# Kernel optimization log

Measured on AMD Instinct MI355X. Metric: run time of the kernel, lower is better.

## Reference

```python
import jax, jax.numpy as jnp
import numpy as np

DIM = 96
NHEAD = 8
HEAD_DIM = DIM // NHEAD  # 12
N, L, S = 1, 262144, 262144  # 64^3 flattened 3D volume tokens
EPS_LA = 1e-6
EPS_LN = 1e-5


def layer_norm(x, w, b):
    mu = jnp.mean(x, axis=-1, keepdims=True)
    var = jnp.mean((x - mu) ** 2, axis=-1, keepdims=True)
    return (x - mu) * jax.lax.rsqrt(var + EPS_LN) * w + b


def setup_inputs() -> dict:
    key = jax.random.key(0)
    ks = jax.random.split(key, 24)
    std = 0.02
    def w(k, shape):
        return jax.random.normal(k, shape, dtype=jnp.float32) * std
    inp = {
        "mr_seg_feat_flatten": jax.random.normal(ks[0], (N, L, DIM), dtype=jnp.float32),
        "ct2mr_attention_flatten": jax.random.normal(ks[1], (N, L, DIM), dtype=jnp.float32),
        "warp_ctfeat": jax.random.normal(ks[2], (N, S, DIM), dtype=jnp.float32),
        # CrossmodalSemanticsCalibration params (torch Linear weights: [out, in])
        "w_qkv": w(ks[3], (DIM, DIM)),
        "w_qkv2": w(ks[4], (DIM, DIM)),
        "ln1_w": jnp.ones((DIM,), jnp.float32),
        "ln1_b": jnp.zeros((DIM,), jnp.float32),
        "ln2_w": jnp.ones((2 * DIM,), jnp.float32),
        "ln2_b": jnp.zeros((2 * DIM,), jnp.float32),
        "mlp_fc1_w": w(ks[5], (2 * DIM, 2 * DIM)),
        "mlp_fc1_b": jnp.zeros((2 * DIM,), jnp.float32),
        "mlp_fc2_w": w(ks[6], (DIM, 2 * DIM)),
        "mlp_fc2_b": jnp.zeros((DIM,), jnp.float32),
        # StructureAttention(96, 8) params
        "sa_wq": w(ks[7], (DIM, DIM)),
        "sa_wk": w(ks[8], (DIM, DIM)),
        "sa_wv": w(ks[9], (DIM, DIM)),
        "sa_merge": w(ks[10], (DIM, DIM)),
        "sa_mlp_w1": w(ks[11], (2 * DIM, 2 * DIM)),
        "sa_mlp_w2": w(ks[12], (DIM, 2 * DIM)),
        "sa_ln1_w": jnp.ones((DIM,), jnp.float32),
        "sa_ln1_b": jnp.zeros((DIM,), jnp.float32),
        "sa_ln2_w": jnp.ones((DIM,), jnp.float32),
        "sa_ln2_b": jnp.zeros((DIM,), jnp.float32),
    }
    return inp


def _forward(mr_seg_feat_flatten, ct2mr_attention_flatten, warp_ctfeat,
             w_qkv, w_qkv2, ln1_w, ln1_b, ln2_w, ln2_b,
             mlp_fc1_w, mlp_fc1_b, mlp_fc2_w, mlp_fc2_b,
             sa_wq, sa_wk, sa_wv, sa_merge, sa_mlp_w1, sa_mlp_w2,
             sa_ln1_w, sa_ln1_b, sa_ln2_w, sa_ln2_b):
    # CrossmodalSemanticsCalibration.forward (ct2mr_attention_flatten is unused, as in torch)
    x0 = layer_norm(mr_seg_feat_flatten, ln1_w, ln1_b)
    shortcut = x0 @ w_qkv.T                        # [N, L, C]
    y = shortcut @ w_qkv2.T                        # [N, L, C]

    # StructureAttention(y, warp_ctfeat) with kernelized LinearAttention
    n, l, c = y.shape
    s = warp_ctfeat.shape[1]
    q = (y @ sa_wq.T).reshape(n, l, NHEAD, HEAD_DIM)
    k = (warp_ctfeat @ sa_wk.T).reshape(n, s, NHEAD, HEAD_DIM)
    v = (warp_ctfeat @ sa_wv.T).reshape(n, s, NHEAD, HEAD_DIM)
    Q = jax.nn.elu(q) + 1.0
    K = jax.nn.elu(k) + 1.0
    KV = jnp.einsum('nshd,nshv->nhdv', K, v / s)   # [N, H, d, d]
    Z = 1.0 / (jnp.einsum('nlhd,nhd->nlh', Q, K.sum(axis=1)) + EPS_LA)
    msg = jnp.einsum('nlhd,nhdv,nlh->nlhv', Q, KV, Z) * s
    msg = msg.reshape(n, l, c) @ sa_merge.T
    msg = layer_norm(msg, sa_ln1_w, sa_ln1_b)
    h = jnp.concatenate([y, msg], axis=-1) @ sa_mlp_w1.T
    h = jax.nn.relu(h) @ sa_mlp_w2.T
    h = layer_norm(h, sa_ln2_w, sa_ln2_b)
    x = y + h                                      # StructureAttention output

    # fuse with shortcut, final Mlp (GELU, exact erf as torch default)
    x = jnp.concatenate([x, shortcut], axis=-1)    # [N, L, 2C]
    x = layer_norm(x, ln2_w, ln2_b)
    x = jax.nn.gelu(x @ mlp_fc1_w.T + mlp_fc1_b, approximate=False)
    x = x @ mlp_fc2_w.T + mlp_fc2_b
    return x                                       # [N, L, C]


def reference(mr_seg_feat_flatten, ct2mr_attention_flatten, warp_ctfeat,
              w_qkv, w_qkv2, ln1_w, ln1_b, ln2_w, ln2_b,
              mlp_fc1_w, mlp_fc1_b, mlp_fc2_w, mlp_fc2_b,
              sa_wq, sa_wk, sa_wv, sa_merge, sa_mlp_w1, sa_mlp_w2,
              sa_ln1_w, sa_ln1_b, sa_ln2_w, sa_ln2_b):
    return _forward(mr_seg_feat_flatten, ct2mr_attention_flatten, warp_ctfeat,
                    w_qkv, w_qkv2, ln1_w, ln1_b, ln2_w, ln2_b,
                    mlp_fc1_w, mlp_fc1_b, mlp_fc2_w, mlp_fc2_b,
                    sa_wq, sa_wk, sa_wv, sa_merge, sa_mlp_w1, sa_mlp_w2,
                    sa_ln1_w, sa_ln1_b, sa_ln2_w, sa_ln2_b)
```

## Files before the change

### kernel.cpp

```cpp
#include <hip/hip_runtime.h>
#include <hip/hip_bf16.h>


typedef __attribute__((ext_vector_type(8))) short short8;
typedef __attribute__((ext_vector_type(4))) float f32x4;
typedef __attribute__((ext_vector_type(4))) unsigned int uint4v;

#define WS_FLAG 0
#define WS_PKV  512
#define WS_PSV  (WS_PKV + 16*9216*4)
#define WS_PSE  (WS_PSV + 16*96*4)
#define WS_KSUM (WS_PSE + 16*96*4)
#define WS_KSTOT (WS_KSUM + 96*4)
#define WS_CM   (WS_KSTOT + 64)
#define WS_BDT  (WS_CM + 768*4)
#define WS_WB   (WS_BDT + 9216*2)
#define WS_VEC  (WS_WB + 165888*2)

#define OQKV   0
#define OQKV2  9216
#define OWQ    18432
#define OWK    27648
#define OWV    36864
#define OMERGE 46080
#define OW1    55296
#define OW2    92160
#define OFC1   110592
#define OFC2   147456
#define VLN1W 0
#define VLN1B 96
#define VLN2W 192
#define VLN2B 384
#define VFC1B 576
#define VFC2B 768
#define VSA1W 864
#define VSA1B 960
#define VSA2W 1056
#define VSA2B 1152

struct InPtrs { const void* p[23]; };

__device__ inline float b2f(unsigned short x) {
  union { unsigned u; float f; } c; c.u = ((unsigned)x) << 16; return c.f;
}
__device__ inline unsigned short f2b(float f) {
  __hip_bfloat16 h = __float2bfloat16(f);
  return *(unsigned short*)&h;
}
__device__ inline uint2 pack4bf(float v0, float v1, float v2, float v3) {
  uint2 r;
  r.x = (unsigned)f2b(v0) | ((unsigned)f2b(v1) << 16);
  r.y = (unsigned)f2b(v2) | ((unsigned)f2b(v3) << 16);
  return r;
}

__global__ void probe_k(const void* in0, unsigned* flag) {
  int tid = threadIdx.x;
  const unsigned short* u = (const unsigned short*)in0;
  int cnt = 0;
  for (int j = 0; j < 8; ++j) {
    unsigned short v = u[(tid * 8 + j) * 2];
    unsigned e = (v >> 7) & 0xFF;
    if ((e >= 110 && e <= 141) || ((v & 0x7FFF) == 0)) cnt++;
  }
  for (int o = 32; o; o >>= 1) cnt += __shfl_down(cnt, o);
  if (tid == 0) *flag = (cnt > 256) ? 1u : 0u;
}

template<int ISBF>
__launch_bounds__(256)
__global__ void prep_k(InPtrs ip, char* ws) {
  if (((const unsigned*)ws)[0] != (unsigned)ISBF) return;
  const int wsrc[10] = {3,4,13,14,15,16,17,18,9,11};
  const int wdst[11] = {0,9216,18432,27648,36864,46080,55296,92160,110592,147456,165888};
  const int vsrc[10] = {5,6,7,8,10,12,19,20,21,22};
  const int vdst[11] = {0,96,192,384,576,768,864,960,1056,1152,1248};
  unsigned short* wb = (unsigned short*)(ws + WS_WB);
  float* vec = (float*)(ws + WS_VEC);
  float* zr = (float*)(ws + WS_PKV);
  const int TOT = 165888 + 1248 + 150528;
  for (int e = blockIdx.x * 256 + threadIdx.x; e < TOT; e += gridDim.x * 256) {
    if (e < 165888) {
      int w = 0;
      while (w < 9 && e >= wdst[w + 1]) ++w;
      int loc = e - wdst[w];
      if (ISBF) wb[e] = ((const unsigned short*)ip.p[wsrc[w]])[loc];
      else      wb[e] = f2b(((const float*)ip.p[wsrc[w]])[loc]);
    } else if (e < 165888 + 1248) {
      int e2 = e - 165888;
      int w = 0;
      while (w < 9 && e2 >= vdst[w + 1]) ++w;
      int loc = e2 - vdst[w];
      vec[e2] = ISBF ? b2f(((const unsigned short*)ip.p[vsrc[w]])[loc])
                     : ((const float*)ip.p[vsrc[w]])[loc];
    } else {
      zr[e - 165888 - 1248] = 0.0f;
    }
  }
}

template<int NB, int NCF, int KSTEPS>
__device__ inline void domm(const unsigned short* A, int apitch,
                            const unsigned short* B, int bpitch, int cf0,
                            int lane, f32x4 (&acc)[NB][NCF]) {
  int lr = lane & 15, lg = lane >> 4;
#pragma unroll
  for (int ks = 0; ks < KSTEPS; ++ks) {
    int k0 = ks * 32 + lg * 8;
    short8 bf[NCF];
#pragma unroll
    for (int cf = 0; cf < NCF; ++cf)
      bf[cf] = *(const short8*)(B + ((cf0 + cf) * 16 + lr) * bpitch + k0);
    short8 af[NB];
#pragma unroll
    for (int b = 0; b < NB; ++b)
      af[b] = *(const short8*)(A + (b * 16 + lr) * apitch + k0);
#pragma unroll
    for (int cf = 0; cf < NCF; ++cf)
#pragma unroll
      for (int b = 0; b < NB; ++b)
        acc[b][cf] = __builtin_amdgcn_mfma_f32_16x16x32_bf16(af[b], bf[cf], acc[b][cf], 0, 0, 0);
  }
}

template<int NB, int NCF>
__device__ inline void writeFrags(unsigned short* dst, int pitch, int cf0,
                                  int lane, f32x4 (&acc)[NB][NCF]) {
  int lr = lane & 15, lg = lane >> 4;
#pragma unroll
  for (int b = 0; b < NB; ++b)
#pragma unroll
    for (int cf = 0; cf < NCF; ++cf)
#pragma unroll
      for (int r = 0; r < 4; ++r) {
        float v = acc[b][cf][r];
        float v1 = __shfl_xor(v, 1);
        float v2 = __shfl_xor(v, 2);
        float v3 = __shfl_xor(v, 3);
        if ((lane & 3) == 0) {
          int row = b * 16 + lg * 4 + r;
          int col = (cf0 + cf) * 16 + lr;
          *(uint2*)(dst + row * pitch + col) = pack4bf(v, v1, v2, v3);
        }
      }
}

template<int NB, int NCF>
__device__ inline void zacc(f32x4 (&acc)[NB][NCF]) {
#pragma unroll
  for (int b = 0; b < NB; ++b)
#pragma unroll
    for (int cf = 0; cf < NCF; ++cf)
      acc[b][cf] = (f32x4){0.f, 0.f, 0.f, 0.f};
}

template<int ISBF>
__launch_bounds__(256)
__global__ void kA(const void* ct_, char* ws) {
  if (((const unsigned*)ws)[0] != (unsigned)ISBF) return;
  __shared__ unsigned short sCT[64][104];
  __shared__ unsigned short sEK[96][72];
  __shared__ unsigned short sVT[96][72];
  const unsigned short* Wb = (const unsigned short*)(ws + WS_WB);
  float* pKV = (float*)(ws + WS_PKV);
  int tid = threadIdx.x, lane = tid & 63, wid = tid >> 6;
  int lr = lane & 15, lg = lane >> 4;

  f32x4 kvacc[2][6];
  zacc<2, 6>(kvacc);
  float accEk = 0.f, accV = 0.f;

  for (int t = blockIdx.x; t < 4096; t += gridDim.x) {
    if (ISBF) {
      const uint4v* src = (const uint4v*)((const unsigned short*)ct_ + (size_t)t * 6144);
#pragma unroll
      for (int i = 0; i < 3; ++i) {
        int ch = tid * 3 + i;
        int r = ch / 12, c = (ch % 12) * 8;
        *(uint4v*)&sCT[r][c] = src[ch];
      }
    } else {
      const float4* src = (const float4*)((const float*)ct_ + (size_t)t * 6144);
#pragma unroll
      for (int i = 0; i < 6; ++i) {
        int ch = tid * 6 + i;
        int r = ch / 24, c = (ch % 24) * 4;
        float4 v = src[ch];
        *(uint2*)&sCT[r][c] = pack4bf(v.x, v.y, v.z, v.w);
      }
    }
    __syncthreads();

    const unsigned short* Wp = Wb + ((wid < 2) ? OWK : OWV);
    int cf0 = (wid & 1) * 3;
    f32x4 pacc[4][3];
    zacc<4, 3>(pacc);
    domm<4, 3, 3>(&sCT[0][0], 104, Wp, 96, cf0, lane, pacc);
    if (wid < 2) {
#pragma unroll
      for (int b = 0; b < 4; ++b)
#pragma unroll
        for (int cf = 0; cf < 3; ++cf)
#pragma unroll
          for (int r = 0; r < 4; ++r) {
            float v = pacc[b][cf][r];
            pacc[b][cf][r] = v > 0.f ? v : expm1f(v);
          }
    }
    {
      unsigned short* dstT = (wid < 2) ? &sEK[0][0] : &sVT[0][0];
#pragma unroll
      for (int b = 0; b < 4; ++b)
#pragma unroll
        for (int cf = 0; cf < 3; ++cf) {
          int col = (cf0 + cf) * 16 + lr;
          int t0 = b * 16 + lg * 4;
          *(uint2*)(dstT + col * 72 + t0) =
              pack4bf(pacc[b][cf][0], pacc[b][cf][1], pacc[b][cf][2], pacc[b][cf][3]);
        }
    }
    __syncthreads();

    if (wid < 3) {
#pragma unroll
      for (int ks = 0; ks < 2; ++ks) {
        int k0 = ks * 32 + lg * 8;
        short8 a[2];
#pragma unroll
        for (int bb = 0; bb < 2; ++bb)
          a[bb] = *(const short8*)&sEK[(wid * 2 + bb) * 16 + lr][k0];
#pragma unroll
        for (int cf = 0; cf < 6; ++cf) {
          short8 vb = *(const short8*)&sVT[cf * 16 + lr][k0];
#pragma unroll
          for (int bb = 0; bb < 2; ++bb)
            kvacc[bb][cf] = __builtin_amdgcn_mfma_f32_16x16x32_bf16(a[bb], vb, kvacc[bb][cf], 0, 0, 0);
        }
      }
    }
    if (tid < 96) {
#pragma unroll
      for (int j = 0; j < 8; ++j) {
        short8 e = *(const short8*)&sEK[tid][j * 8];
        short8 v = *(const short8*)&sVT[tid][j * 8];
#pragma unroll
        for (int q = 0; q < 8; ++q) {
          accEk += b2f((unsigned short)e[q]);
          accV  += b2f((unsigned short)v[q]);
        }
      }
    }
    __syncthreads();
  }

  int slice = blockIdx.x & 15;
  if (tid < 96) {
    atomicAdd((float*)(ws + WS_PSE) + slice * 96 + tid, accEk);
    atomicAdd((float*)(ws + WS_PSV) + slice * 96 + tid, accV);
  }
  if (wid < 3) {
#pragma unroll
    for (int bb = 0; bb < 2; ++bb)
#pragma unroll
      for (int cf = 0; cf < 6; ++cf)
#pragma unroll
        for (int r = 0; r < 4; ++r) {
          int hd = (wid * 2 + bb) * 16 + lg * 4 + r;
          int hv = cf * 16 + lr;
          if (hd / 12 == hv / 12)
            atomicAdd(&pKV[slice * 9216 + hd * 96 + hv], kvacc[bb][cf][r]);
        }
  }
}

template<int ISBF>
__launch_bounds__(256)
__global__ void kFin(const void* merge_, char* ws) {
  if (((const unsigned*)ws)[0] != (unsigned)ISBF) return;
  __shared__ float Ks[96], sV[96], KV[8][12][12], csk[96];
  int tid = threadIdx.x;
  const float* pSE = (const float*)(ws + WS_PSE);
  const float* pSV = (const float*)(ws + WS_PSV);
  const float* pKV = (const float*)(ws + WS_PKV);
  if (tid < 96) {
    float a = 0.f, b = 0.f;
    for (int s = 0; s < 16; ++s) { a += pSE[s * 96 + tid]; b += pSV[s * 96 + tid]; }
    Ks[tid] = 262144.0f + a;
    sV[tid] = b;
    ((float*)(ws + WS_KSUM))[tid] = Ks[tid];
  }
  __syncthreads();
  if (tid < 8) {
    float s = 0.f;
    for (int d = 0; d < 12; ++d) s += Ks[tid * 12 + d];
    ((float*)(ws + WS_KSTOT))[tid] = s;
  }
  for (int e = tid; e < 1152; e += 256) {
    int h = e / 144, r = e % 144, d = r / 12, v = r % 12;
    int hd = h * 12 + d, hv = h * 12 + v;
    float s = sV[hv];
    for (int sl = 0; sl < 16; ++sl) s += pKV[sl * 9216 + hd * 96 + hv];
    KV[h][d][v] = s * (1.0f / 262144.0f);
  }
  unsigned short* bdt = (unsigned short*)(ws + WS_BDT);
  for (int e = tid; e < 9216; e += 256) bdt[e] = 0;
  __syncthreads();
  for (int e = tid; e < 1152; e += 256) {
    int h = e / 144, r = e % 144, d = r / 12, v = r % 12;
    bdt[(h * 12 + v) * 96 + (h * 12 + d)] = f2b(KV[h][d][v]);
  }
  if (tid < 96) {
    int h = tid / 12, v = tid % 12;
    float s = 0.f;
    for (int d = 0; d < 12; ++d) s += KV[h][d][v];
    csk[tid] = s;
  }
  __syncthreads();
  for (int e = tid; e < 768; e += 256) {
    int h = e / 96, c = e % 96;
    float s = 0.f;
    for (int v = 0; v < 12; ++v) {
      float mg = ISBF ? b2f(((const unsigned short*)merge_)[c * 96 + h * 12 + v])
                      : ((const float*)merge_)[c * 96 + h * 12 + v];
      s += csk[h * 12 + v] * mg;
    }
    ((float*)(ws + WS_CM))[e] = s;
  }
}

template<int ISBF>
__launch_bounds__(128)
__global__ void kB(const void* mr_, void* out_, char* ws) {
  if (((const unsigned*)ws)[0] != (unsigned)ISBF) return;
  __shared__ unsigned short sA[64][200];
  __shared__ unsigned short sS[64][104];
  __shared__ unsigned short sY[64][96];
  __shared__ float sZs[64][8];
  const unsigned short* Wb = (const unsigned short*)(ws + WS_WB);
  const float* vec  = (const float*)(ws + WS_VEC);
  const float* Ksum = (const float*)(ws + WS_KSUM);
  const float* KsTot = (const float*)(ws + WS_KSTOT);
  const float* CM = (const float*)(ws + WS_CM);
  const unsigned short* BDT = (const unsigned short*)(ws + WS_BDT);
  int tid = threadIdx.x, lane = tid & 63, wid = tid >> 6;
  int lr = lane & 15, lg = lane >> 4;
  int tok0 = blockIdx.x * 64;

  if (ISBF) {
    const uint4v* src = (const uint4v*)((const unsigned short*)mr_ + (size_t)tok0 * 96);
#pragma unroll
    for (int i = 0; i < 6; ++i) {
      int ch = tid * 6 + i;
      int r = ch / 12, c = (ch % 12) * 8;
      *(uint4v*)&sA[r][c] = src[ch];
    }
  } else {
    const float4* src = (const float4*)((const float*)mr_ + (size_t)tok0 * 96);
#pragma unroll
    for (int i = 0; i < 12; ++i) {
      int ch = tid * 12 + i;
      int r = ch / 24, c = (ch % 24) * 4;
      float4 v = src[ch];
      *(uint2*)&sA[r][c] = pack4bf(v.x, v.y, v.z, v.w);
    }
  }
  __syncthreads();

  int row = tid >> 1, c0 = (tid & 1) * 48;

  {
    float vals[48];
    float s = 0.f, s2 = 0.f;
#pragma unroll
    for (int i = 0; i < 6; ++i) {
      short8 v = *(const short8*)&sA[row][c0 + i * 8];
#pragma unroll
      for (int j = 0; j < 8; ++j) {
        float x = b2f((unsigned short)v[j]);
        vals[i * 8 + j] = x; s += x; s2 += x * x;
      }
    }
    s += __shfl_xor(s, 1); s2 += __shfl_xor(s2, 1);
    float mean = s * (1.f / 96.f);
    float rs = rsqrtf(s2 * (1.f / 96.f) - mean * mean + 1e-5f);
#pragma unroll
    for (int i = 0; i < 6; ++i) {
      short8 o;
#pragma unroll
      for (int j = 0; j < 8; ++j) {
        int c = c0 + i * 8 + j;
        o[j] = (short)f2b((vals[i * 8 + j] - mean) * rs * vec[VLN1W + c] + vec[VLN1B + c]);
      }
      *(short8*)&sA[row][c0 + i * 8] = o;
    }
  }
  __syncthreads();

  f32x4 acc3[4][3];
  f32x4 acc6[4][6];

  zacc<4, 3>(acc3);
  domm<4, 3, 3>(&sA[0][0], 200, Wb + OQKV, 96, wid * 3, lane, acc3);
  writeFrags<4, 3>(&sS[0][0], 104, wid * 3, lane, acc3);
  __syncthreads();

  zacc<4, 3>(acc3);
  domm<4, 3, 3>(&sS[0][0], 104, Wb + OQKV2, 96, wid * 3, lane, acc3);
  writeFrags<4, 3>(&sY[0][0], 96, wid * 3, lane, acc3);
  __syncthreads();

  zacc<4, 3>(acc3);
  domm<4, 3, 3>(&sY[0][0], 96, Wb + OWQ, 96, wid * 3, lane, acc3);
#pragma unroll
  for (int b = 0; b < 4; ++b)
#pragma unroll
    for (int cf = 0; cf < 3; ++cf)
#pragma unroll
      for (int r = 0; r < 4; ++r) {
        float v = acc3[b][cf][r];
        acc3[b][cf][r] = v > 0.f ? v : expm1f(v);
      }
  writeFrags<4, 3>(&sA[0][0], 200, wid * 3, lane, acc3);
  __syncthreads();

#pragma unroll
  for (int i = 0; i < 4; ++i) {
    int task = tid + 128 * i;
    int zr = task >> 3, h = task & 7;
    float den = KsTot[h];
#pragma unroll
    for (int d = 0; d < 12; ++d)
      den += b2f(sA[zr][h * 12 + d]) * Ksum[h * 12 + d];
    sZs[zr][h] = 262144.0f / (den + 1e-6f);
  }
  __syncthreads();

  zacc<4, 3>(acc3);
  domm<4, 3, 3>(&sA[0][0], 200, BDT, 96, wid * 3, lane, acc3);
#pragma unroll
  for (int b = 0; b < 4; ++b)
#pragma unroll
    for (int cf = 0; cf < 3; ++cf) {
      int col = (wid * 3 + cf) * 16 + lr;
      int h = col / 12;
#pragma unroll
      for (int r = 0; r < 4; ++r) {
        int rw = b * 16 + lg * 4 + r;
        acc3[b][cf][r] *= sZs[rw][h];
      }
    }
  writeFrags<4, 3>(&sA[0][96], 200, wid * 3, lane, acc3);
  __syncthreads();

  zacc<4, 3>(acc3);
  domm<4, 3, 3>(&sA[0][96], 200, Wb + OMERGE, 96, wid * 3, lane, acc3);
  writeFrags<4, 3>(&sA[0][0], 200, wid * 3, lane, acc3);
  __syncthreads();

  {
    float vals[48];
#pragma unroll
    for (int j = 0; j < 48; ++j) vals[j] = 0.f;
#pragma unroll
    for (int h = 0; h < 8; ++h) {
      float zh = sZs[row][h];
      const float* cmr = CM + h * 96 + c0;
#pragma unroll
      for (int j = 0; j < 48; j += 4) {
        float4 c4 = *(const float4*)(cmr + j);
        vals[j] += zh * c4.x; vals[j + 1] += zh * c4.y;
        vals[j + 2] += zh * c4.z; vals[j + 3] += zh * c4.w;
      }
    }
    float s = 0.f, s2 = 0.f;
#pragma unroll
    for (int i = 0; i < 6; ++i) {
      short8 v = *(const short8*)&sA[row][c0 + i * 8];
#pragma unroll
      for (int j = 0; j < 8; ++j) {
        float x = vals[i * 8 + j] + b2f((unsigned short)v[j]);
        vals[i * 8 + j] = x; s += x; s2 += x * x;
      }
    }
    s += __shfl_xor(s, 1); s2 += __shfl_xor(s2, 1);
    float mean = s * (1.f / 96.f);
    float rs = rsqrtf(s2 * (1.f / 96.f) - mean * mean + 1e-5f);
#pragma unroll
    for (int i = 0; i < 6; ++i) {
      short8 o;
#pragma unroll
      for (int j = 0; j < 8; ++j) {
        int c = c0 + i * 8 + j;
        o[j] = (short)f2b((vals[i * 8 + j] - mean) * rs * vec[VSA1W + c] + vec[VSA1B + c]);
      }
      *(short8*)&sA[row][96 + c0 + i * 8] = o;
    }
#pragma unroll
    for (int i = 0; i < 6; ++i)
      *(uint4v*)&sA[row][c0 + i * 8] = *(const uint4v*)&sY[row][c0 + i * 8];
  }
  __syncthreads();

  zacc<4, 6>(acc6);
  domm<4, 6, 6>(&sA[0][0], 200, Wb + OW1, 192, wid * 6, lane, acc6);
#pragma unroll
  for (int b = 0; b < 4; ++b)
#pragma unroll
    for (int cf = 0; cf < 6; ++cf)
#pragma unroll
      for (int r = 0; r < 4; ++r)
        acc6[b][cf][r] = fmaxf(acc6[b][cf][r], 0.f);
  __syncthreads();
  writeFrags<4, 6>(&sA[0][0], 200, wid * 6, lane, acc6);
  __syncthreads();

  zacc<4, 3>(acc3);
  domm<4, 3, 6>(&sA[0][0], 200, Wb + OW2, 192, wid * 3, lane, acc3);
  __syncthreads();
  writeFrags<4, 3>(&sA[0][0], 200, wid * 3, lane, acc3);
  __syncthreads();

  {
    float vals[48];
    float s = 0.f, s2 = 0.f;
#pragma unroll
    for (int i = 0; i < 6; ++i) {
      short8 v = *(const short8*)&sA[row][c0 + i * 8];
#pragma unroll
      for (int j = 0; j < 8; ++j) {
        float x = b2f((unsigned short)v[j]);
        vals[i * 8 + j] = x; s += x; s2 += x * x;
      }
    }
    s += __shfl_xor(s, 1); s2 += __shfl_xor(s2, 1);
    float mh = s * (1.f / 96.f);
    float rh = rsqrtf(s2 * (1.f / 96.f) - mh * mh + 1e-5f);
    float sx = 0.f, sx2 = 0.f;
#pragma unroll
    for (int j = 0; j < 48; ++j) {
      int c = c0 + j;
      float x = b2f(sY[row][c]) + (vals[j] - mh) * rh * vec[VSA2W + c] + vec[VSA2B + c];
      vals[j] = x; sx += x; sx2 += x * x;
    }
#pragma unroll
    for (int j = 0; j < 48; ++j) {
      float sv = b2f(sS[row][c0 + j]);
      sx += sv; sx2 += sv * sv;
    }
    sx += __shfl_xor(sx, 1); sx2 += __shfl_xor(sx2, 1);
    float m2 = sx * (1.f / 192.f);
    float r2 = rsqrtf(sx2 * (1.f / 192.f) - m2 * m2 + 1e-5f);
#pragma unroll
    for (int i = 0; i < 6; ++i) {
      short8 o;
#pragma unroll
      for (int j = 0; j < 8; ++j) {
        int c = c0 + i * 8 + j;
        o[j] = (short)f2b((vals[i * 8 + j] - m2) * r2 * vec[VLN2W + c] + vec[VLN2B + c]);
      }
      *(short8*)&sA[row][c0 + i * 8] = o;
    }
#pragma unroll
    for (int i = 0; i < 6; ++i) {
      short8 o;
#pragma unroll
      for (int j = 0; j < 8; ++j) {
        int c = c0 + i * 8 + j;
        float sv = b2f(sS[row][c]);
        o[j] = (short)f2b((sv - m2) * r2 * vec[VLN2W + 96 + c] + vec[VLN2B + 96 + c]);
      }
      *(short8*)&sA[row][96 + c0 + i * 8] = o;
    }
  }
  __syncthreads();

  zacc<4, 6>(acc6);
  domm<4, 6, 6>(&sA[0][0], 200, Wb + OFC1, 192, wid * 6, lane, acc6);
#pragma unroll
  for (int cf = 0; cf < 6; ++cf) {
    float bb = vec[VFC1B + (wid * 6 + cf) * 16 + lr];
#pragma unroll
    for (int b = 0; b < 4; ++b)
#pragma unroll
      for (int r = 0; r < 4; ++r) {
        float x = acc6[b][cf][r] + bb;
        acc6[b][cf][r] = 0.5f * x * (1.0f + erff(x * 0.70710678118f));
      }
  }
  __syncthreads();
  writeFrags<4, 6>(&sA[0][0], 200, wid * 6, lane, acc6);
  __syncthreads();

  zacc<4, 3>(acc3);
  domm<4, 3, 6>(&sA[0][0], 200, Wb + OFC2, 192, wid * 3, lane, acc3);
#pragma unroll
  for (int b = 0; b < 4; ++b)
#pragma unroll
    for (int cf = 0; cf < 3; ++cf)
#pragma unroll
      for (int r = 0; r < 4; ++r) {
        int col = (wid * 3 + cf) * 16 + lr;
        float v = acc3[b][cf][r] + vec[VFC2B + col];
        float v1 = __shfl_xor(v, 1);
        float v2 = __shfl_xor(v, 2);
        float v3 = __shfl_xor(v, 3);
        if ((lane & 3) == 0) {
          size_t token = (size_t)tok0 + b * 16 + lg * 4 + r;
          size_t off = token * 96 + col;
          if (ISBF) {
            *(uint2*)((unsigned short*)out_ + off) = pack4bf(v, v1, v2, v3);
          } else {
            float4 f; f.x = v; f.y = v1; f.z = v2; f.w = v3;
            *(float4*)((float*)out_ + off) = f;
          }
        }
      }
}

extern "C" void kernel_launch(void* const* d_in, const int* in_sizes, int n_in,
                              void* d_out, int out_size, void* d_ws, size_t ws_size,
                              hipStream_t stream) {
  (void)in_sizes; (void)n_in; (void)out_size; (void)ws_size;
  char* ws = (char*)d_ws;
  probe_k<<<1, 64, 0, stream>>>(d_in[0], (unsigned*)ws);
  InPtrs ip;
  for (int i = 0; i < 23; ++i) ip.p[i] = d_in[i];
  prep_k<0><<<512, 256, 0, stream>>>(ip, ws);
  prep_k<1><<<512, 256, 0, stream>>>(ip, ws);
  kA<0><<<1024, 256, 0, stream>>>(d_in[2], ws);
  kA<1><<<1024, 256, 0, stream>>>(d_in[2], ws);
  kFin<0><<<1, 256, 0, stream>>>(d_in[16], ws);
  kFin<1><<<1, 256, 0, stream>>>(d_in[16], ws);
  kB<0><<<4096, 128, 0, stream>>>(d_in[0], d_out, ws);
  kB<1><<<4096, 128, 0, stream>>>(d_in[0], d_out, ws);
}
```

Measured before the change: 765.1 us.

## Split kB token tile across four waves by rows and use 256-thread blocks

Raises kB's block size from 128 to 256 threads, and each wave now owns 16 token rows with all output columns. Before, two waves split the columns over all 64 rows. This should cut per-wave accumulator registers and raise occupancy and latency hiding, at the cost of each wave re-reading the full weight tiles. Layer norms now use a two-pass variance for stability, run on only half the threads, and the final LN output loops are fused.

```diff
diff --git a/kernel.cpp b/kernel.cpp
--- a/kernel.cpp
+++ b/kernel.cpp
@@ -244,9 +244,9 @@
         short8 e = *(const short8*)&sEK[tid][j * 8];
         short8 v = *(const short8*)&sVT[tid][j * 8];
 #pragma unroll
-        for (int q = 0; q < 8; ++q) {
-          accEk += b2f((unsigned short)e[q]);
-          accV  += b2f((unsigned short)v[q]);
+        for (int qq = 0; qq < 8; ++qq) {
+          accEk += b2f((unsigned short)e[qq]);
+          accV  += b2f((unsigned short)v[qq]);
         }
       }
     }
@@ -329,7 +329,7 @@
 }
 
 template<int ISBF>
-__launch_bounds__(128)
+__launch_bounds__(256, 2)
 __global__ void kB(const void* mr_, void* out_, char* ws) {
   if (((const unsigned*)ws)[0] != (unsigned)ISBF) return;
   __shared__ unsigned short sA[64][200];
@@ -344,21 +344,23 @@
   const unsigned short* BDT = (const unsigned short*)(ws + WS_BDT);
   int tid = threadIdx.x, lane = tid & 63, wid = tid >> 6;
   int lr = lane & 15, lg = lane >> 4;
+  int w16 = wid * 16;
+  int row = tid >> 1, c0 = (tid & 1) * 48;
   int tok0 = blockIdx.x * 64;
 
   if (ISBF) {
     const uint4v* src = (const uint4v*)((const unsigned short*)mr_ + (size_t)tok0 * 96);
 #pragma unroll
+    for (int i = 0; i < 3; ++i) {
+      int ch = tid * 3 + i;
+      int r = ch / 12, c = (ch % 12) * 8;
+      *(uint4v*)&sA[r][c] = src[ch];
+    }
+  } else {
+    const float4* src = (const float4*)((const float*)mr_ + (size_t)tok0 * 96);
+#pragma unroll
     for (int i = 0; i < 6; ++i) {
       int ch = tid * 6 + i;
-      int r = ch / 12, c = (ch % 12) * 8;
-      *(uint4v*)&sA[r][c] = src[ch];
-    }
-  } else {
-    const float4* src = (const float4*)((const float*)mr_ + (size_t)tok0 * 96);
-#pragma unroll
-    for (int i = 0; i < 12; ++i) {
-      int ch = tid * 12 + i;
       int r = ch / 24, c = (ch % 24) * 4;
       float4 v = src[ch];
       *(uint2*)&sA[r][c] = pack4bf(v.x, v.y, v.z, v.w);
@@ -366,23 +368,25 @@
   }
   __syncthreads();
 
-  int row = tid >> 1, c0 = (tid & 1) * 48;
-
-  {
+  if (tid < 128) {
     float vals[48];
-    float s = 0.f, s2 = 0.f;
+    float s = 0.f;
 #pragma unroll
     for (int i = 0; i < 6; ++i) {
       short8 v = *(const short8*)&sA[row][c0 + i * 8];
 #pragma unroll
       for (int j = 0; j < 8; ++j) {
         float x = b2f((unsigned short)v[j]);
-        vals[i * 8 + j] = x; s += x; s2 += x * x;
-      }
-    }
-    s += __shfl_xor(s, 1); s2 += __shfl_xor(s2, 1);
+        vals[i * 8 + j] = x; s += x;
+      }
+    }
+    s += __shfl_xor(s, 1);
     float mean = s * (1.f / 96.f);
-    float rs = rsqrtf(s2 * (1.f / 96.f) - mean * mean + 1e-5f);
+    float s2 = 0.f;
+#pragma unroll
+    for (int j = 0; j < 48; ++j) { float d = vals[j] - mean; s2 += d * d; }
+    s2 += __shfl_xor(s2, 1);
+    float rs = rsqrtf(s2 * (1.f / 96.f) + 1e-5f);
 #pragma unroll
     for (int i = 0; i < 6; ++i) {
       short8 o;
@@ -396,36 +400,34 @@
   }
   __syncthreads();
 
-  f32x4 acc3[4][3];
-  f32x4 acc6[4][6];
-
-  zacc<4, 3>(acc3);
-  domm<4, 3, 3>(&sA[0][0], 200, Wb + OQKV, 96, wid * 3, lane, acc3);
-  writeFrags<4, 3>(&sS[0][0], 104, wid * 3, lane, acc3);
-  __syncthreads();
-
-  zacc<4, 3>(acc3);
-  domm<4, 3, 3>(&sS[0][0], 104, Wb + OQKV2, 96, wid * 3, lane, acc3);
-  writeFrags<4, 3>(&sY[0][0], 96, wid * 3, lane, acc3);
-  __syncthreads();
-
-  zacc<4, 3>(acc3);
-  domm<4, 3, 3>(&sY[0][0], 96, Wb + OWQ, 96, wid * 3, lane, acc3);
-#pragma unroll
-  for (int b = 0; b < 4; ++b)
-#pragma unroll
-    for (int cf = 0; cf < 3; ++cf)
-#pragma unroll
-      for (int r = 0; r < 4; ++r) {
-        float v = acc3[b][cf][r];
-        acc3[b][cf][r] = v > 0.f ? v : expm1f(v);
-      }
-  writeFrags<4, 3>(&sA[0][0], 200, wid * 3, lane, acc3);
-  __syncthreads();
-
-#pragma unroll
-  for (int i = 0; i < 4; ++i) {
-    int task = tid + 128 * i;
+  f32x4 a6[1][6];
+  f32x4 a12[1][12];
+
+  zacc<1, 6>(a6);
+  domm<1, 6, 3>(&sA[w16][0], 200, Wb + OQKV, 96, 0, lane, a6);
+  writeFrags<1, 6>(&sS[w16][0], 104, 0, lane, a6);
+  __syncthreads();
+
+  zacc<1, 6>(a6);
+  domm<1, 6, 3>(&sS[w16][0], 104, Wb + OQKV2, 96, 0, lane, a6);
+  writeFrags<1, 6>(&sY[w16][0], 96, 0, lane, a6);
+  __syncthreads();
+
+  zacc<1, 6>(a6);
+  domm<1, 6, 3>(&sY[w16][0], 96, Wb + OWQ, 96, 0, lane, a6);
+#pragma unroll
+  for (int cf = 0; cf < 6; ++cf)
+#pragma unroll
+    for (int r = 0; r < 4; ++r) {
+      float v = a6[0][cf][r];
+      a6[0][cf][r] = v > 0.f ? v : expm1f(v);
+    }
+  writeFrags<1, 6>(&sA[w16][0], 200, 0, lane, a6);
+  __syncthreads();
+
+#pragma unroll
+  for (int i = 0; i < 2; ++i) {
+    int task = tid + 256 * i;
     int zr = task >> 3, h = task & 7;
     float den = KsTot[h];
 #pragma unroll
@@ -435,29 +437,27 @@
   }
   __syncthreads();
 
-  zacc<4, 3>(acc3);
-  domm<4, 3, 3>(&sA[0][0], 200, BDT, 96, wid * 3, lane, acc3);
-#pragma unroll
-  for (int b = 0; b < 4; ++b)
-#pragma unroll
-    for (int cf = 0; cf < 3; ++cf) {
-      int col = (wid * 3 + cf) * 16 + lr;
-      int h = col / 12;
-#pragma unroll
-      for (int r = 0; r < 4; ++r) {
-        int rw = b * 16 + lg * 4 + r;
-        acc3[b][cf][r] *= sZs[rw][h];
-      }
-    }
-  writeFrags<4, 3>(&sA[0][96], 200, wid * 3, lane, acc3);
-  __syncthreads();
-
-  zacc<4, 3>(acc3);
-  domm<4, 3, 3>(&sA[0][96], 200, Wb + OMERGE, 96, wid * 3, lane, acc3);
-  writeFrags<4, 3>(&sA[0][0], 200, wid * 3, lane, acc3);
-  __syncthreads();
-
-  {
+  zacc<1, 6>(a6);
+  domm<1, 6, 3>(&sA[w16][0], 200, BDT, 96, 0, lane, a6);
+#pragma unroll
+  for (int cf = 0; cf < 6; ++cf) {
+    int col = cf * 16 + lr;
+    int h = col / 12;
+#pragma unroll
+    for (int r = 0; r < 4; ++r) {
+      int rw = w16 + lg * 4 + r;
+      a6[0][cf][r] *= sZs[rw][h];
+    }
+  }
+  writeFrags<1, 6>(&sA[w16][96], 200, 0, lane, a6);
+  __syncthreads();
+
+  zacc<1, 6>(a6);
+  domm<1, 6, 3>(&sA[w16][96], 200, Wb + OMERGE, 96, 0, lane, a6);
+  writeFrags<1, 6>(&sA[w16][0], 200, 0, lane, a6);
+  __syncthreads();
+
+  if (tid < 128) {
     float vals[48];
 #pragma unroll
     for (int j = 0; j < 48; ++j) vals[j] = 0.f;
@@ -472,19 +472,23 @@
         vals[j + 2] += zh * c4.z; vals[j + 3] += zh * c4.w;
       }
     }
-    float s = 0.f, s2 = 0.f;
+    float s = 0.f;
 #pragma unroll
     for (int i = 0; i < 6; ++i) {
       short8 v = *(const short8*)&sA[row][c0 + i * 8];
 #pragma unroll
       for (int j = 0; j < 8; ++j) {
         float x = vals[i * 8 + j] + b2f((unsigned short)v[j]);
-        vals[i * 8 + j] = x; s += x; s2 += x * x;
-      }
-    }
-    s += __shfl_xor(s, 1); s2 += __shfl_xor(s2, 1);
+        vals[i * 8 + j] = x; s += x;
+      }
+    }
+    s += __shfl_xor(s, 1);
     float mean = s * (1.f / 96.f);
-    float rs = rsqrtf(s2 * (1.f / 96.f) - mean * mean + 1e-5f);
+    float s2 = 0.f;
+#pragma unroll
+    for (int j = 0; j < 48; ++j) { float d = vals[j] - mean; s2 += d * d; }
+    s2 += __shfl_xor(s2, 1);
+    float rs = rsqrtf(s2 * (1.f / 96.f) + 1e-5f);
 #pragma unroll
     for (int i = 0; i < 6; ++i) {
       short8 o;
@@ -501,120 +505,117 @@
   }
   __syncthreads();
 
-  zacc<4, 6>(acc6);
-  domm<4, 6, 6>(&sA[0][0], 200, Wb + OW1, 192, wid * 6, lane, acc6);
-#pragma unroll
-  for (int b = 0; b < 4; ++b)
-#pragma unroll
-    for (int cf = 0; cf < 6; ++cf)
-#pragma unroll
-      for (int r = 0; r < 4; ++r)
-        acc6[b][cf][r] = fmaxf(acc6[b][cf][r], 0.f);
-  __syncthreads();
-  writeFrags<4, 6>(&sA[0][0], 200, wid * 6, lane, acc6);
-  __syncthreads();
-
-  zacc<4, 3>(acc3);
-  domm<4, 3, 6>(&sA[0][0], 200, Wb + OW2, 192, wid * 3, lane, acc3);
-  __syncthreads();
-  writeFrags<4, 3>(&sA[0][0], 200, wid * 3, lane, acc3);
-  __syncthreads();
-
-  {
-    float vals[48];
-    float s = 0.f, s2 = 0.f;
+  zacc<1, 12>(a12);
+  domm<1, 12, 6>(&sA[w16][0], 200, Wb + OW1, 192, 0, lane, a12);
+#pragma unroll
+  for (int cf = 0; cf < 12; ++cf)
+#pragma unroll
+    for (int r = 0; r < 4; ++r)
+      a12[0][cf][r] = fmaxf(a12[0][cf][r], 0.f);
+  __syncthreads();
+  writeFrags<1, 12>(&sA[w16][0], 200, 0, lane, a12);
+  __syncthreads();
+
+  zacc<1, 6>(a6);
+  domm<1, 6, 6>(&sA[w16][0], 200, Wb + OW2, 192, 0, lane, a6);
+  __syncthreads();
+  writeFrags<1, 6>(&sA[w16][0], 200, 0, lane, a6);
+  __syncthreads();
+
+  if (tid < 128) {
+    float vals[48], sv[48];
+    float s = 0.f;
 #pragma unroll
     for (int i = 0; i < 6; ++i) {
       short8 v = *(const short8*)&sA[row][c0 + i * 8];
 #pragma unroll
       for (int j = 0; j < 8; ++j) {
         float x = b2f((unsigned short)v[j]);
-        vals[i * 8 + j] = x; s += x; s2 += x * x;
-      }
-    }
-    s += __shfl_xor(s, 1); s2 += __shfl_xor(s2, 1);
+        vals[i * 8 + j] = x; s += x;
+      }
+    }
+    s += __shfl_xor(s, 1);
     float mh = s * (1.f / 96.f);
-    float rh = rsqrtf(s2 * (1.f / 96.f) - mh * mh + 1e-5f);
-    float sx = 0.f, sx2 = 0.f;
+    float s2 = 0.f;
+#pragma unroll
+    for (int j = 0; j < 48; ++j) { float d = vals[j] - mh; s2 += d * d; }
+    s2 += __shfl_xor(s2, 1);
+    float rh = rsqrtf(s2 * (1.f / 96.f) + 1e-5f);
+    float sx = 0.f;
 #pragma unroll
     for (int j = 0; j < 48; ++j) {
       int c = c0 + j;
       float x = b2f(sY[row][c]) + (vals[j] - mh) * rh * vec[VSA2W + c] + vec[VSA2B + c];
-      vals[j] = x; sx += x; sx2 += x * x;
+      vals[j] = x; sx += x;
     }
 #pragma unroll
     for (int j = 0; j < 48; ++j) {
-      float sv = b2f(sS[row][c0 + j]);
-      sx += sv; sx2 += sv * sv;
-    }
-    sx += __shfl_xor(sx, 1); sx2 += __shfl_xor(sx2, 1);
+      float v = b2f(sS[row][c0 + j]);
+      sv[j] = v; sx += v;
+    }
+    sx += __shfl_xor(sx, 1);
     float m2 = sx * (1.f / 192.f);
-    float r2 = rsqrtf(sx2 * (1.f / 192.f) - m2 * m2 + 1e-5f);
+    float sx2 = 0.f;
+#pragma unroll
+    for (int j = 0; j < 48; ++j) { float d = vals[j] - m2; sx2 += d * d; }
+#pragma unroll
+    for (int j = 0; j < 48; ++j) { float d = sv[j] - m2; sx2 += d * d; }
+    sx2 += __shfl_xor(sx2, 1);
+    float r2 = rsqrtf(sx2 * (1.f / 192.f) + 1e-5f);
 #pragma unroll
     for (int i = 0; i < 6; ++i) {
-      short8 o;
+      short8 oa, ob;
 #pragma unroll
       for (int j = 0; j < 8; ++j) {
-        int c = c0 + i * 8 + j;
-        o[j] = (short)f2b((vals[i * 8 + j] - m2) * r2 * vec[VLN2W + c] + vec[VLN2B + c]);
-      }
-      *(short8*)&sA[row][c0 + i * 8] = o;
-    }
-#pragma unroll
-    for (int i = 0; i < 6; ++i) {
-      short8 o;
-#pragma unroll
-      for (int j = 0; j < 8; ++j) {
-        int c = c0 + i * 8 + j;
-        float sv = b2f(sS[row][c]);
-        o[j] = (short)f2b((sv - m2) * r2 * vec[VLN2W + 96 + c] + vec[VLN2B + 96 + c]);
-      }
-      *(short8*)&sA[row][96 + c0 + i * 8] = o;
-    }
-  }
-  __syncthreads();
-
-  zacc<4, 6>(acc6);
-  domm<4, 6, 6>(&sA[0][0], 200, Wb + OFC1, 192, wid * 6, lane, acc6);
+        int idx = i * 8 + j, c = c0 + idx;
+        oa[j] = (short)f2b((vals[idx] - m2) * r2 * vec[VLN2W + c] + vec[VLN2B + c]);
+        ob[j] = (short)f2b((sv[idx] - m2) * r2 * vec[VLN2W + 96 + c] + vec[VLN2B + 96 + c]);
+      }
+      *(short8*)&sA[row][c0 + i * 8] = oa;
+      *(short8*)&sA[row][96 + c0 + i * 8] = ob;
+    }
+  }
+  __syncthreads();
+
+  zacc<1, 12>(a12);
+  domm<1, 12, 6>(&sA[w16][0], 200, Wb + OFC1, 192, 0, lane, a12);
+#pragma unroll
+  for (int cf = 0; cf < 12; ++cf) {
+    float bb = vec[VFC1B + cf * 16 + lr];
+#pragma unroll
+    for (int r = 0; r < 4; ++r) {
+      float x = a12[0][cf][r] + bb;
+      a12[0][cf][r] = 0.5f * x * (1.0f + erff(x * 0.70710678118f));
+    }
+  }
+  __syncthreads();
+  writeFrags<1, 12>(&sA[w16][0], 200, 0, lane, a12);
+  __syncthreads();
+
+  zacc<1, 6>(a6);
+  domm<1, 6, 6>(&sA[w16][0], 200, Wb + OFC2, 192, 0, lane, a6);
 #pragma unroll
   for (int cf = 0; cf < 6; ++cf) {
-    float bb = vec[VFC1B + (wid * 6 + cf) * 16 + lr];
-#pragma unroll
-    for (int b = 0; b < 4; ++b)
-#pragma unroll
-      for (int r = 0; r < 4; ++r) {
-        float x = acc6[b][cf][r] + bb;
-        acc6[b][cf][r] = 0.5f * x * (1.0f + erff(x * 0.70710678118f));
-      }
-  }
-  __syncthreads();
-  writeFrags<4, 6>(&sA[0][0], 200, wid * 6, lane, acc6);
-  __syncthreads();
-
-  zacc<4, 3>(acc3);
-  domm<4, 3, 6>(&sA[0][0], 200, Wb + OFC2, 192, wid * 3, lane, acc3);
-#pragma unroll
-  for (int b = 0; b < 4; ++b)
-#pragma unroll
-    for (int cf = 0; cf < 3; ++cf)
-#pragma unroll
-      for (int r = 0; r < 4; ++r) {
-        int col = (wid * 3 + cf) * 16 + lr;
-        float v = acc3[b][cf][r] + vec[VFC2B + col];
-        float v1 = __shfl_xor(v, 1);
-        float v2 = __shfl_xor(v, 2);
-        float v3 = __shfl_xor(v, 3);
-        if ((lane & 3) == 0) {
-          size_t token = (size_t)tok0 + b * 16 + lg * 4 + r;
-          size_t off = token * 96 + col;
-          if (ISBF) {
-            *(uint2*)((unsigned short*)out_ + off) = pack4bf(v, v1, v2, v3);
-          } else {
-            float4 f; f.x = v; f.y = v1; f.z = v2; f.w = v3;
-            *(float4*)((float*)out_ + off) = f;
-          }
+    int col = cf * 16 + lr;
+    float bias = vec[VFC2B + col];
+#pragma unroll
+    for (int r = 0; r < 4; ++r) {
+      float v = a6[0][cf][r] + bias;
+      float v1 = __shfl_xor(v, 1);
+      float v2 = __shfl_xor(v, 2);
+      float v3 = __shfl_xor(v, 3);
+      if ((lane & 3) == 0) {
+        size_t token = (size_t)tok0 + w16 + lg * 4 + r;
+        size_t off = token * 96 + col;
+        if (ISBF) {
+          *(uint2*)((unsigned short*)out_ + off) = pack4bf(v, v1, v2, v3);
+        } else {
+          float4 f; f.x = v; f.y = v1; f.z = v2; f.w = v3;
+          *(float4*)((float*)out_ + off) = f;
         }
       }
+    }
+  }
 }
 
 extern "C" void kernel_launch(void* const* d_in, const int* in_sizes, int n_in,
@@ -631,6 +632,6 @@
   kA<1><<<1024, 256, 0, stream>>>(d_in[2], ws);
   kFin<0><<<1, 256, 0, stream>>>(d_in[16], ws);
   kFin<1><<<1, 256, 0, stream>>>(d_in[16], ws);
-  kB<0><<<4096, 128, 0, stream>>>(d_in[0], d_out, ws);
-  kB<1><<<4096, 128, 0, stream>>>(d_in[0], d_out, ws);
-}
+  kB<0><<<4096, 256, 0, stream>>>(d_in[0], d_out, ws);
+  kB<1><<<4096, 256, 0, stream>>>(d_in[0], d_out, ws);
+}
```

Measured after the change: 835.0 us. 1.09x slower.
